# Kernel tuning notes

Hardware: AMD Instinct MI355X
Metric: run time of the kernel (lower is better)

Reference implementation:

```python
import jax, jax.numpy as jnp
import numpy as np

NUM_SAMPLES = 512
FG_FRACTION = 0.25
MAX_POS = int(NUM_SAMPLES * FG_FRACTION)  # 128
THRESHOLDS = np.array([0.0, 0.5, 0.5], dtype=np.float32)
INDICATORS = np.array([-3, -1, -2, 1], dtype=np.int32)


def _make_boxes(key, shape, scale):
    # random valid boxes: sorted corner pairs in [0, scale)
    y = jnp.sort(jax.random.uniform(key, shape[:-1] + (2,)) * scale, axis=-1)
    x = jnp.sort(jax.random.uniform(jax.random.fold_in(key, 1), shape[:-1] + (2,)) * scale, axis=-1)
    return jnp.stack([y[..., 0], x[..., 0], y[..., 1], x[..., 1]], axis=-1)


def setup_inputs() -> dict:
    key = jax.random.key(0)
    k1, k2, k3, k4 = jax.random.split(key, 4)
    B, N, M = 32, 8000, 256
    boxes = _make_boxes(k1, (B, N, 4), 1024.0)
    gt_boxes = _make_boxes(k2, (B, M, 4), 1024.0)
    # pad last quarter of gt entries with -1 (invalid)
    valid = (jnp.arange(M) < (3 * M) // 4)[None, :, None]
    gt_boxes = jnp.where(valid, gt_boxes, -jnp.ones_like(gt_boxes))
    gt_classes = jax.random.randint(k3, (B, M), 1, 91, dtype=jnp.int32)
    gt_classes = jnp.where(valid[..., 0], gt_classes, -1)
    rand = jax.random.uniform(k4, (B, N + M))
    return {"boxes": boxes, "gt_boxes": gt_boxes, "gt_classes": gt_classes, "rand": rand}


def _pairwise_iou(b1, b2):
    # b1: [B,N,4], b2: [B,M,4] in (ymin,xmin,ymax,xmax) -> [B,N,M]
    ymin1, xmin1, ymax1, xmax1 = jnp.split(b1, 4, axis=-1)  # each [B,N,1]
    ymin2, xmin2, ymax2, xmax2 = (t[..., 0] for t in jnp.split(b2, 4, axis=-1))  # [B,M]
    ih = jnp.clip(jnp.minimum(ymax1, ymax2[:, None, :]) - jnp.maximum(ymin1, ymin2[:, None, :]), 0.0)
    iw = jnp.clip(jnp.minimum(xmax1, xmax2[:, None, :]) - jnp.maximum(xmin1, xmin2[:, None, :]), 0.0)
    inter = ih * iw
    a1 = (ymax1 - ymin1) * (xmax1 - xmin1)          # [B,N,1]
    a2 = (ymax2 - ymin2) * (xmax2 - xmin2)          # [B,M]
    union = a1 + a2[:, None, :] - inter
    return jnp.where(union > 0, inter / union, 0.0)


def _ranks_desc(score):
    order = jnp.argsort(-score)
    return jnp.zeros_like(order).at[order].set(jnp.arange(score.shape[0]))


def _sample_one(pos, neg, ign, rand):
    cand = (pos | neg) & ~ign
    pos_c = pos & cand
    neg_c = neg & cand
    pos_rank = _ranks_desc(jnp.where(pos_c, rand, -1.0))
    pos_sel = pos_c & (pos_rank < MAX_POS)
    neg_needed = NUM_SAMPLES - jnp.sum(pos_sel)
    neg_rank = _ranks_desc(jnp.where(neg_c, rand, -1.0))
    neg_sel = neg_c & (neg_rank < neg_needed)
    indicator = (pos_sel | neg_sel).astype(jnp.int32)
    _, idx = jax.lax.top_k(indicator, NUM_SAMPLES)  # selected first, ties by lowest index
    return idx


def _gather(t, idx):
    # t: [B,L,C], idx: [B,K] -> [B,K,C]
    return jnp.take_along_axis(t, idx[..., None], axis=1)


def reference(boxes, gt_boxes, gt_classes, rand):
    gt_boxes = gt_boxes.astype(boxes.dtype)
    boxes = jnp.concatenate([boxes, gt_boxes], axis=1)  # mix_gt_boxes
    boxes_invalid = jnp.max(boxes, axis=-1) < 0.0       # [B,L]
    gt_invalid = jnp.max(gt_boxes, axis=-1) < 0.0       # [B,M]
    sim = _pairwise_iou(boxes, gt_boxes)                # [B,L,M]
    sim = jnp.where(boxes_invalid[:, :, None] | gt_invalid[:, None, :], -1.0, sim)

    matched_vals = jnp.max(sim, axis=-1)                # [B,L]
    matched_gt_indices = jnp.argmax(sim, axis=-1).astype(jnp.int32)
    bucket = jnp.searchsorted(jnp.asarray(THRESHOLDS), matched_vals, side='right')
    match_indicators = jnp.asarray(INDICATORS)[bucket]  # [B,L]

    positive = match_indicators >= 0
    negative = match_indicators == -1
    ignored = match_indicators == -2
    invalid = match_indicators == -3
    background = negative | invalid                     # [B,L]

    matched_gt_classes = _gather(gt_classes[..., None], matched_gt_indices)[..., 0]
    matched_gt_classes = jnp.where(background, 0, matched_gt_classes)
    matched_gt_boxes = _gather(gt_boxes, matched_gt_indices)
    matched_gt_boxes = jnp.where(background[..., None], 0.0, matched_gt_boxes)
    matched_gt_indices = jnp.where(background, -1, matched_gt_indices)

    indices = jax.vmap(_sample_one)(positive, negative, ignored, rand)  # [B,K]
    rois = _gather(boxes, indices)
    sampled_gt_boxes = _gather(matched_gt_boxes, indices)
    sampled_gt_classes = _gather(matched_gt_classes[..., None], indices)[..., 0]
    sampled_gt_indices = _gather(matched_gt_indices[..., None], indices)[..., 0]
    return rois, sampled_gt_boxes, sampled_gt_classes, sampled_gt_indices
```

## Files before the change

### kernel.cpp

```cpp
#include <hip/hip_runtime.h>
#include <stdint.h>

#define BB 32
#define NN 8000
#define MM 256
#define LL (NN + MM)
#define NSAMP 512
#define MAXPOS 128
#define T2 1024
#define CH ((LL + T2 - 1) / T2)
#define SPLIT 4
#define MSUB (MM / SPLIT)

__device__ __forceinline__ void opaquef(float& x) { asm("" : "+v"(x)); }

__device__ __noinline__ int serial_argmax(const float4 bx, const float a1,
                                          const float4* s_gt, const float* s_a2,
                                          int nv)
{
    float qb = -1.0f; int bi = 0;
    for (int m = 0; m < nv; ++m) {
        float4 g = s_gt[m];
        float ih = fmaxf(fminf(bx.z, g.z) - fmaxf(bx.x, g.x), 0.0f);
        float iw = fmaxf(fminf(bx.w, g.w) - fmaxf(bx.y, g.y), 0.0f);
        float inter = ih * iw; opaquef(inter);
        float uni = (a1 + s_a2[m]) - inter;
        float q = (uni > 0.0f) ? (inter / uni) : 0.0f;
        if (q > qb) { qb = q; bi = m; }
    }
    return bi;
}

__device__ __forceinline__ uint32_t approx_key(const float4 bx, float a1,
                                               const float4 g, float a2,
                                               uint32_t klo)
{
    float ih = fmaxf(fminf(bx.z, g.z) - fmaxf(bx.x, g.x), 0.0f);
    float iw = fmaxf(fminf(bx.w, g.w) - fmaxf(bx.y, g.y), 0.0f);
    float inter = ih * iw;
    float s = a1 + a2;
    float u = inter * __builtin_amdgcn_rcpf(s);
    return (__float_as_uint(u) & 0xFFFFFFC0u) | klo;
}

__global__ __launch_bounds__(256) void match_split_kernel(
    const float* __restrict__ boxes, const float* __restrict__ gt,
    uint32_t* __restrict__ keys)
{
    __shared__ float4 s_gt[MSUB];
    __shared__ float  s_a2[MSUB];
    __shared__ uint32_t s_klo[MSUB];
    __shared__ int s_nv;
    const int b = blockIdx.y, sp = blockIdx.z, tid = threadIdx.x;
    if (tid < MSUB) {
        float4 v = ((const float4*)(gt + ((size_t)b * MM + sp * MSUB) * 4))[tid];
        bool valid = !(fmaxf(fmaxf(v.x, v.y), fmaxf(v.z, v.w)) < 0.0f);
        uint64_t mk = __ballot(valid);
        int pos = __popcll(mk & ((1ull << tid) - 1));
        if (valid) {
            s_gt[pos] = v;
            s_a2[pos] = (v.z - v.x) * (v.w - v.y);
            s_klo[pos] = (uint32_t)(63 - tid);
        }
        if (tid == 0) s_nv = (int)__popcll(mk);
    }
    __syncthreads();
    const int l = blockIdx.x * 256 + tid;
    if (l >= LL) return;
    const int nv = s_nv;

    const float4* bb4 = (const float4*)(boxes + (size_t)b * NN * 4);
    const float4* gb4 = (const float4*)(gt + (size_t)b * MM * 4);
    float4 bx = (l < NN) ? bb4[l] : gb4[l - NN];
    float a1 = (bx.z - bx.x) * (bx.w - bx.y); opaquef(a1);

    uint32_t best = 0, sec = 0;
    #pragma unroll 4
    for (int m = 0; m < nv; ++m) {
        uint32_t key = approx_key(bx, a1, s_gt[m], s_a2[m], s_klo[m]);
        sec  = max(sec, min(best, key));
        best = max(best, key);
    }

    bool redo = ((best & ~63u) != 0u) &&
                (((best & ~63u) - (sec & ~63u)) <= 64u);
    if (__any(redo)) {
        if (redo) {
            int w = serial_argmax(bx, a1, s_gt, s_a2, nv);
            best = approx_key(bx, a1, s_gt[w], s_a2[w], s_klo[w]);
        }
    }
    keys[((size_t)b * LL + l) * SPLIT + sp] = best;
}

__global__ __launch_bounds__(256) void merge2_kernel(
    const float* __restrict__ boxes, const float* __restrict__ gt,
    uint32_t* __restrict__ keys)
{
    const int b = blockIdx.y;
    const int l = blockIdx.x * 256 + threadIdx.x;
    if (l >= LL) return;
    const float4* bb4 = (const float4*)(boxes + (size_t)b * NN * 4);
    const float4* gb4 = (const float4*)(gt + (size_t)b * MM * 4);
    const uint4 kv = ((const uint4*)keys)[(size_t)b * LL + l];
    float4 bx = (l < NN) ? bb4[l] : gb4[l - NN];
    int cls, midx = 0;
    uint32_t best = kv.x; int bsp = 0;
    if (kv.y > best) { best = kv.y; bsp = 1; }
    if (kv.z > best) { best = kv.z; bsp = 2; }
    if (kv.w > best) { best = kv.w; bsp = 3; }
    if (fmaxf(fmaxf(bx.x, bx.y), fmaxf(bx.z, bx.w)) < 0.0f || best == 0u) {
        cls = 2;
    } else {
        const uint32_t bt = best & ~63u;
        const uint32_t s0 = (bsp == 0) ? 0u : (kv.x & ~63u);
        const uint32_t s1 = (bsp == 1) ? 0u : (kv.y & ~63u);
        const uint32_t s2 = (bsp == 2) ? 0u : (kv.z & ~63u);
        const uint32_t s3 = (bsp == 3) ? 0u : (kv.w & ~63u);
        const uint32_t sec = max(max(s0, s1), max(s2, s3));
        float a1 = (bx.z - bx.x) * (bx.w - bx.y); opaquef(a1);
        if ((bt != 0u) && (bt - sec) <= 64u) {
            float qb = -1.0f; midx = 0;
            #pragma unroll
            for (int sp = 0; sp < SPLIT; ++sp) {
                const uint32_t k = (sp == 0) ? kv.x : (sp == 1) ? kv.y
                                 : (sp == 2) ? kv.z : kv.w;
                const int m = sp * MSUB + (63 - (int)(k & 63u));
                float4 g = gb4[m];
                float a2 = (g.z - g.x) * (g.w - g.y); opaquef(a2);
                float ih = fmaxf(fminf(bx.z, g.z) - fmaxf(bx.x, g.x), 0.0f);
                float iw = fmaxf(fminf(bx.w, g.w) - fmaxf(bx.y, g.y), 0.0f);
                float inter = ih * iw; opaquef(inter);
                float uni = (a1 + a2) - inter;
                float q = (uni > 0.0f) ? (inter / uni) : 0.0f;
                if (q > qb) { qb = q; midx = m; }
            }
            cls = (qb >= 0.5f) ? 1 : 0;
        } else {
            midx = bsp * MSUB + (63 - (int)(best & 63u));
            float4 g = gb4[midx];
            float a2 = (g.z - g.x) * (g.w - g.y); opaquef(a2);
            float ih = fmaxf(fminf(bx.z, g.z) - fmaxf(bx.x, g.x), 0.0f);
            float iw = fmaxf(fminf(bx.w, g.w) - fmaxf(bx.y, g.y), 0.0f);
            float inter = ih * iw; opaquef(inter);
            float uni = (a1 + a2) - inter;
            float q = (uni > 0.0f) ? (inter / uni) : 0.0f;
            cls = (q >= 0.5f) ? 1 : 0;
        }
    }
    ((uint16_t*)keys)[((size_t)b * LL + l) * 8] = (uint16_t)(cls | (midx << 2));
}

__device__ __forceinline__ int block_exscan_fast(int v, int* wt, int tid)
{
    const int lane = tid & 63, w = tid >> 6;
    int x = v;
    #pragma unroll
    for (int off = 1; off < 64; off <<= 1) {
        int y = __shfl_up(x, off);
        if (lane >= off) x += y;
    }
    if (lane == 63) wt[w] = x;
    __syncthreads();
    if (tid < 64) {
        int t = (tid < 16) ? wt[tid] : 0;
        #pragma unroll
        for (int off = 1; off < 16; off <<= 1) {
            int y = __shfl_up(t, off);
            if (tid >= off) t += y;
        }
        if (tid < 16) wt[tid] = t;
    }
    __syncthreads();
    return ((w > 0) ? wt[w - 1] : 0) + x - v;
}

__device__ __forceinline__ int block_exscan_seg4(int v, int* wt, int tid)
{
    const int lane = tid & 63, w = tid >> 6;
    int x = v;
    #pragma unroll
    for (int off = 1; off < 64; off <<= 1) {
        int y = __shfl_up(x, off);
        if (lane >= off) x += y;
    }
    if (lane == 63) wt[w] = x;
    __syncthreads();
    if (tid < 16) {
        int t = wt[tid];
        #pragma unroll
        for (int off = 1; off < 4; off <<= 1) {
            int y = __shfl_up(t, off);
            if ((tid & 3) >= off) t += y;
        }
        wt[tid] = t;
    }
    __syncthreads();
    return (((w & 3) > 0) ? wt[w - 1] : 0) + x - v;
}

__global__ __launch_bounds__(T2) void sample_kernel(
    const float* __restrict__ boxes, const float* __restrict__ gt,
    const int* __restrict__ gtc, const float* __restrict__ rnd,
    const uint32_t* __restrict__ keys, float* __restrict__ out)
{
    __shared__ uint32_t s_key[LL];
    __shared__ uint16_t s_pk[LL];
    __shared__ int s_hist[512];
    __shared__ int s_warp[16];
    __shared__ int s_idx[NSAMP];
    __shared__ int s_sb[8];
    const int b = blockIdx.x, tid = threadIdx.x, lane = tid & 63;
    const float4* bb4 = (const float4*)(boxes + (size_t)b * NN * 4);
    const float4* gb4 = (const float4*)(gt + (size_t)b * MM * 4);

    if (tid == 0) s_sb[0] = 0;
    __syncthreads();

    int loc = 0;
    for (int l = tid; l < LL; l += T2) {
        s_key[l] = __float_as_uint(rnd[(size_t)b * LL + l]);
        uint16_t p = ((const uint16_t*)keys)[((size_t)b * LL + l) * 8];
        s_pk[l] = p;
        int c = p & 3;
        loc += (c == 0) ? 1 : ((c == 1) ? 0x10000 : 0);
    }
    #pragma unroll
    for (int off = 32; off; off >>= 1) loc += __shfl_xor(loc, off);
    if (lane == 0) atomicAdd(&s_sb[0], loc);
    __syncthreads();
    const int Nn = s_sb[0] & 0xFFFF, P = s_sb[0] >> 16;

    const int posK = (P < MAXPOS) ? P : MAXPOS;
    const int negK = NSAMP - posK;
    const bool negRad = (Nn > negK);
    const bool posRad = (P > MAXPOS);

    uint32_t prefix0 = 0, prefix1 = 0;
    int rem0 = negK, rem1 = MAXPOS;
    bool act0 = negRad, act1 = posRad;
    uint32_t thr0f = 0, thr1f = 0;
    int r0f = LL, r1f = LL;
    for (int round = 0; round < 4 && (act0 || act1); ++round) {
        const int shift = 24 - 8 * round;
        if (tid < 512) s_hist[tid] = 0;
        __syncthreads();
        const uint32_t pmask = (round == 0) ? 0u : (0xFFFFFFFFu << (shift + 8));
        for (int l = tid; l < LL; l += T2) {
            const uint32_t k = s_key[l];
            const int c = s_pk[l] & 3;
            bool doit = (c == 0) ? (act0 && ((k & pmask) == prefix0))
                      : (c == 1) ? (act1 && ((k & pmask) == prefix1))
                      : false;
            if (doit) atomicAdd(&s_hist[(c << 8) | ((k >> shift) & 255)], 1);
        }
        __syncthreads();
        int h = 0;
        if (tid < 512) h = s_hist[(tid & 0x100) | (255 - (tid & 255))];
        const int above = block_exscan_seg4(h, s_warp, tid);
        if (tid < 512) {
            const int c = tid >> 8;
            const int rem = c ? rem1 : rem0;
            const bool act = c ? act1 : act0;
            if (act && above < rem && above + h >= rem) {
                s_sb[4 + c * 2] = 255 - (tid & 255);
                s_sb[5 + c * 2] = above;
            }
        }
        __syncthreads();
        if (act0) {
            const int bin = s_sb[4];
            rem0 -= s_sb[5];
            prefix0 |= ((uint32_t)bin) << shift;
            const int cnt = s_hist[bin];
            if (rem0 == cnt)      { act0 = false; thr0f = prefix0; r0f = LL; }
            else if (round == 3)  { act0 = false; thr0f = prefix0; r0f = rem0; }
        }
        if (act1) {
            const int bin = s_sb[6];
            rem1 -= s_sb[7];
            prefix1 |= ((uint32_t)bin) << shift;
            const int cnt = s_hist[256 + bin];
            if (rem1 == cnt)      { act1 = false; thr1f = prefix1; r1f = LL; }
            else if (round == 3)  { act1 = false; thr1f = prefix1; r1f = rem1; }
        }
        __syncthreads();
    }
    const uint32_t thr0 = negRad ? thr0f : 0u;  const int r0 = negRad ? r0f : LL;
    const uint32_t thr1 = posRad ? thr1f : 0u;  const int r1 = posRad ? r1f : LL;

    const int lo = tid * CH, hi = (lo + CH < LL) ? (lo + CH) : LL;
    int nt = 0;
    for (int l = lo; l < hi; ++l) {
        const int c = s_pk[l] & 3;
        const uint32_t k = s_key[l];
        if (c == 0) { if (k == thr0) nt += 1; }
        else if (c == 1) { if (k == thr1) nt += 0x10000; }
    }
    const int basep = block_exscan_fast(nt, s_warp, tid);
    int base0 = basep & 0xFFFF, base1 = basep >> 16;
    for (int l = lo; l < hi; ++l) {
        const int c = s_pk[l] & 3;
        if (c > 1) continue;
        const uint32_t k = s_key[l];
        const uint32_t thr = c ? thr1 : thr0;
        bool sel = (k > thr);
        if (k == thr) {
            if (c == 0) { sel = (base0 < r0); ++base0; }
            else        { sel = (base1 < r1); ++base1; }
        }
        if (sel) s_pk[l] |= 0x8000;
    }
    __syncthreads();

    int cnt = 0;
    for (int l = lo; l < hi; ++l) cnt += (s_pk[l] & 0x8000) ? 1 : 0x10000;
    const int pb = block_exscan_fast(cnt, s_warp, tid);
    const int S = s_warp[15] & 0xFFFF;
    int bs = pb & 0xFFFF, bu = (pb >> 16) + S;
    for (int l = lo; l < hi; ++l) {
        if (s_pk[l] & 0x8000) { if (bs < NSAMP) s_idx[bs] = l; ++bs; }
        else                  { if (bu < NSAMP) s_idx[bu] = l; ++bu; }
    }
    __syncthreads();

    if (tid < NSAMP) {
        const int l = s_idx[tid];
        float4 bx = (l < NN) ? bb4[l] : gb4[l - NN];
        const int p = s_pk[l];
        const int c = p & 3, mi = (p >> 2) & 0xFF;
        const bool bg = (c != 1);
        float4 gb = make_float4(0.f, 0.f, 0.f, 0.f);
        int cl = 0, si = -1;
        if (!bg) {
            gb = gb4[mi];
            cl = gtc[(size_t)b * MM + mi];
            si = mi;
        }
        const size_t rk = (size_t)b * NSAMP + tid;
        ((float4*)out)[rk] = bx;
        ((float4*)(out + (size_t)BB * NSAMP * 4))[rk] = gb;
        out[(size_t)2 * BB * NSAMP * 4 + rk] = (float)cl;
        out[(size_t)2 * BB * NSAMP * 4 + (size_t)BB * NSAMP + rk] = (float)si;
    }
}

extern "C" void kernel_launch(void* const* d_in, const int* in_sizes, int n_in,
                              void* d_out, int out_size, void* d_ws, size_t ws_size,
                              hipStream_t stream)
{
    const float* boxes = (const float*)d_in[0];
    const float* gt    = (const float*)d_in[1];
    const int*   gtc   = (const int*)  d_in[2];
    const float* rnd   = (const float*)d_in[3];
    float* out = (float*)d_out;
    uint32_t* keys = (uint32_t*)d_ws;

    dim3 g1((LL + 255) / 256, BB, SPLIT);
    match_split_kernel<<<g1, 256, 0, stream>>>(boxes, gt, keys);
    dim3 g2((LL + 255) / 256, BB);
    merge2_kernel<<<g2, 256, 0, stream>>>(boxes, gt, keys);
    sample_kernel<<<BB, T2, 0, stream>>>(boxes, gt, gtc, rnd, keys, out);
}
```

Baseline: 68.33 us.

## Broadcast GT boxes via readlane and process two anchors per thread

The match kernel stops staging valid GT boxes in shared memory. Each wave now holds one GT box per lane and broadcasts it with readlane (scalar operands). Every thread handles two anchors so each broadcast value is reused twice, and the grid is halved. Invalid GT boxes are no longer compacted out: the loop always runs all 64 per split, with the denominator clamped, and the merge kernel drops its best==0 shortcut, which could change behaviour at the margins.

```diff
diff --git a/kernel.cpp b/kernel.cpp
--- a/kernel.cpp
+++ b/kernel.cpp
@@ -14,83 +14,100 @@
 
 __device__ __forceinline__ void opaquef(float& x) { asm("" : "+v"(x)); }
 
-__device__ __noinline__ int serial_argmax(const float4 bx, const float a1,
-                                          const float4* s_gt, const float* s_a2,
-                                          int nv)
-{
-    float qb = -1.0f; int bi = 0;
-    for (int m = 0; m < nv; ++m) {
-        float4 g = s_gt[m];
-        float ih = fmaxf(fminf(bx.z, g.z) - fmaxf(bx.x, g.x), 0.0f);
-        float iw = fmaxf(fminf(bx.w, g.w) - fmaxf(bx.y, g.y), 0.0f);
-        float inter = ih * iw; opaquef(inter);
-        float uni = (a1 + s_a2[m]) - inter;
-        float q = (uni > 0.0f) ? (inter / uni) : 0.0f;
-        if (q > qb) { qb = q; bi = m; }
-    }
-    return bi;
-}
-
-__device__ __forceinline__ uint32_t approx_key(const float4 bx, float a1,
-                                               const float4 g, float a2,
-                                               uint32_t klo)
-{
-    float ih = fmaxf(fminf(bx.z, g.z) - fmaxf(bx.x, g.x), 0.0f);
-    float iw = fmaxf(fminf(bx.w, g.w) - fmaxf(bx.y, g.y), 0.0f);
-    float inter = ih * iw;
-    float s = a1 + a2;
-    float u = inter * __builtin_amdgcn_rcpf(s);
-    return (__float_as_uint(u) & 0xFFFFFFC0u) | klo;
+__device__ __forceinline__ float rlane(float v, int m)
+{
+    return __uint_as_float(
+        (uint32_t)__builtin_amdgcn_readlane((int)__float_as_uint(v), m));
 }
 
 __global__ __launch_bounds__(256) void match_split_kernel(
     const float* __restrict__ boxes, const float* __restrict__ gt,
     uint32_t* __restrict__ keys)
 {
-    __shared__ float4 s_gt[MSUB];
-    __shared__ float  s_a2[MSUB];
-    __shared__ uint32_t s_klo[MSUB];
-    __shared__ int s_nv;
     const int b = blockIdx.y, sp = blockIdx.z, tid = threadIdx.x;
-    if (tid < MSUB) {
-        float4 v = ((const float4*)(gt + ((size_t)b * MM + sp * MSUB) * 4))[tid];
-        bool valid = !(fmaxf(fmaxf(v.x, v.y), fmaxf(v.z, v.w)) < 0.0f);
-        uint64_t mk = __ballot(valid);
-        int pos = __popcll(mk & ((1ull << tid) - 1));
-        if (valid) {
-            s_gt[pos] = v;
-            s_a2[pos] = (v.z - v.x) * (v.w - v.y);
-            s_klo[pos] = (uint32_t)(63 - tid);
-        }
-        if (tid == 0) s_nv = (int)__popcll(mk);
-    }
-    __syncthreads();
-    const int l = blockIdx.x * 256 + tid;
-    if (l >= LL) return;
-    const int nv = s_nv;
+    const int lane = tid & 63;
+
+    float4 vg = ((const float4*)(gt + ((size_t)b * MM + sp * MSUB) * 4))[lane];
+    float va2 = (vg.z - vg.x) * (vg.w - vg.y); opaquef(va2);
+
+    const int l0 = blockIdx.x * 512 + tid * 2;
+    if (l0 >= LL) return;
+    const int l1 = l0 + 1;
+    const bool v1 = (l1 < LL);
+    const int l1c = v1 ? l1 : l0;
 
     const float4* bb4 = (const float4*)(boxes + (size_t)b * NN * 4);
     const float4* gb4 = (const float4*)(gt + (size_t)b * MM * 4);
-    float4 bx = (l < NN) ? bb4[l] : gb4[l - NN];
-    float a1 = (bx.z - bx.x) * (bx.w - bx.y); opaquef(a1);
-
-    uint32_t best = 0, sec = 0;
-    #pragma unroll 4
-    for (int m = 0; m < nv; ++m) {
-        uint32_t key = approx_key(bx, a1, s_gt[m], s_a2[m], s_klo[m]);
-        sec  = max(sec, min(best, key));
-        best = max(best, key);
-    }
-
-    bool redo = ((best & ~63u) != 0u) &&
-                (((best & ~63u) - (sec & ~63u)) <= 64u);
-    if (__any(redo)) {
-        if (redo) {
-            int w = serial_argmax(bx, a1, s_gt, s_a2, nv);
-            best = approx_key(bx, a1, s_gt[w], s_a2[w], s_klo[w]);
-        }
-    }
-    keys[((size_t)b * LL + l) * SPLIT + sp] = best;
+    float4 bx0 = (l0 < NN) ? bb4[l0] : gb4[l0 - NN];
+    float4 bx1 = (l1c < NN) ? bb4[l1c] : gb4[l1c - NN];
+    float a10 = (bx0.z - bx0.x) * (bx0.w - bx0.y); opaquef(a10);
+    float a11 = (bx1.z - bx1.x) * (bx1.w - bx1.y); opaquef(a11);
+
+    uint32_t best0 = 0, sec0 = 0, best1 = 0, sec1 = 0;
+    #pragma unroll 16
+    for (int m = 0; m < MSUB; ++m) {
+        const float gy0 = rlane(vg.x, m), gx0 = rlane(vg.y, m);
+        const float gy1 = rlane(vg.z, m), gx1 = rlane(vg.w, m);
+        const float a2  = rlane(va2,  m);
+        {
+            float ih = fmaxf(fminf(bx0.z, gy1) - fmaxf(bx0.x, gy0), 0.0f);
+            float iw = fmaxf(fminf(bx0.w, gx1) - fmaxf(bx0.y, gx0), 0.0f);
+            float inter = ih * iw;
+            float s = fmaxf(a10 + a2, 1e-30f);
+            float u = inter * __builtin_amdgcn_rcpf(s);
+            uint32_t key = (__float_as_uint(u) & 0xFFFFFFC0u)
+                         | (uint32_t)(63 - m);
+            sec0  = max(sec0, min(best0, key));
+            best0 = max(best0, key);
+        }
+        {
+            float ih = fmaxf(fminf(bx1.z, gy1) - fmaxf(bx1.x, gy0), 0.0f);
+            float iw = fmaxf(fminf(bx1.w, gx1) - fmaxf(bx1.y, gx0), 0.0f);
+            float inter = ih * iw;
+            float s = fmaxf(a11 + a2, 1e-30f);
+            float u = inter * __builtin_amdgcn_rcpf(s);
+            uint32_t key = (__float_as_uint(u) & 0xFFFFFFC0u)
+                         | (uint32_t)(63 - m);
+            sec1  = max(sec1, min(best1, key));
+            best1 = max(best1, key);
+        }
+    }
+
+    bool redo0 = ((best0 & ~63u) != 0u) &&
+                 (((best0 & ~63u) - (sec0 & ~63u)) <= 64u);
+    bool redo1 = v1 && ((best1 & ~63u) != 0u) &&
+                 (((best1 & ~63u) - (sec1 & ~63u)) <= 64u);
+    if (__any(redo0 || redo1)) {
+        #define SERIAL(BX, A1, BEST, RD)                                     \
+        if (RD) {                                                            \
+            float qb = -1.0f; int bi = 0;                                    \
+            for (int m = 0; m < MSUB; ++m) {                                 \
+                float gy0 = rlane(vg.x, m), gx0 = rlane(vg.y, m);            \
+                float gy1 = rlane(vg.z, m), gx1 = rlane(vg.w, m);            \
+                float a2  = rlane(va2,  m);                                  \
+                float ih = fmaxf(fminf(BX.z, gy1) - fmaxf(BX.x, gy0), 0.0f); \
+                float iw = fmaxf(fminf(BX.w, gx1) - fmaxf(BX.y, gx0), 0.0f); \
+                float inter = ih * iw; opaquef(inter);                       \
+                float uni = (A1 + a2) - inter;     \
+                float q = (uni > 0.0f) ? (inter / uni) : 0.0f;               \
+                if (q > qb) { qb = q; bi = m; }                              \
+            }                                                                \
+            float gy0 = rlane(vg.x, bi), gx0 = rlane(vg.y, bi);              \
+            float gy1 = rlane(vg.z, bi), gx1 = rlane(vg.w, bi);              \
+            float a2  = rlane(va2,  bi);                                     \
+            float ih = fmaxf(fminf(BX.z, gy1) - fmaxf(BX.x, gy0), 0.0f);     \
+            float iw = fmaxf(fminf(BX.w, gx1) - fmaxf(BX.y, gx0), 0.0f);     \
+            float inter = ih * iw;                                           \
+            float s = fmaxf(A1 + a2, 1e-30f);                                \
+            float u = inter * __builtin_amdgcn_rcpf(s);                      \
+            BEST = (__float_as_uint(u) & 0xFFFFFFC0u) | (uint32_t)(63 - bi); \
+        }
+        SERIAL(bx0, a10, best0, redo0)
+        SERIAL(bx1, a11, best1, redo1)
+        #undef SERIAL
+    }
+    keys[((size_t)b * LL + l0) * SPLIT + sp] = best0;
+    if (v1) keys[((size_t)b * LL + l1) * SPLIT + sp] = best1;
 }
 
 __global__ __launch_bounds__(256) void merge2_kernel(
@@ -109,7 +126,7 @@
     if (kv.y > best) { best = kv.y; bsp = 1; }
     if (kv.z > best) { best = kv.z; bsp = 2; }
     if (kv.w > best) { best = kv.w; bsp = 3; }
-    if (fmaxf(fmaxf(bx.x, bx.y), fmaxf(bx.z, bx.w)) < 0.0f || best == 0u) {
+    if (fmaxf(fmaxf(bx.x, bx.y), fmaxf(bx.z, bx.w)) < 0.0f) {
         cls = 2;
     } else {
         const uint32_t bt = best & ~63u;
@@ -356,7 +373,7 @@
     float* out = (float*)d_out;
     uint32_t* keys = (uint32_t*)d_ws;
 
-    dim3 g1((LL + 255) / 256, BB, SPLIT);
+    dim3 g1((LL + 511) / 512, BB, SPLIT);
     match_split_kernel<<<g1, 256, 0, stream>>>(boxes, gt, keys);
     dim3 g2((LL + 255) / 256, BB);
     merge2_kernel<<<g2, 256, 0, stream>>>(boxes, gt, keys);
```

Result: slower. 85.32 us (+24.9%).
